# Kernel optimization log

Hardware: AMD Instinct MI355X
Metric: run time of the kernel (lower is better)

The kernel has to match this reference:

```python
import jax, jax.numpy as jnp
import numpy as np

N_NODES = 50000
N_EDGES = 800000
IN_DIM = 128
HIDDEN_DIMS = [128, 128]
OUT_DIM = 4
NUM_GRAPHS = 128


def setup_inputs() -> dict:
    key = jax.random.key(0)
    ks = jax.random.split(key, 12)
    inp = {
        "x": jax.random.normal(ks[0], (N_NODES, IN_DIM), dtype=jnp.float32),
        "edge_index": jax.random.randint(ks[1], (2, N_EDGES), 0, N_NODES, dtype=jnp.int64),
        "edge_attr": jax.random.uniform(ks[2], (N_EDGES,), dtype=jnp.float32),
        "edge_weight": jax.random.uniform(ks[3], (N_EDGES,), dtype=jnp.float32),
        "batch": jnp.sort(jax.random.randint(ks[4], (N_NODES,), 0, NUM_GRAPHS, dtype=jnp.int64)),
    }
    # GCNConv weights (Glorot-ish scale) and biases
    d_in = IN_DIM
    for i, d_out in enumerate(HIDDEN_DIMS):
        inp[f"W{i}"] = jax.random.normal(ks[5 + i], (d_in, d_out), dtype=jnp.float32) / np.sqrt(d_in)
        inp[f"b{i}"] = jnp.zeros((d_out,), dtype=jnp.float32)
        d_in = d_out
    # classifier: Linear(d,d) -> ReLU -> Linear(d,4)
    inp["Wc1"] = jax.random.normal(ks[8], (d_in, d_in), dtype=jnp.float32) / np.sqrt(d_in)
    inp["bc1"] = jnp.zeros((d_in,), dtype=jnp.float32)
    inp["Wc2"] = jax.random.normal(ks[9], (d_in, OUT_DIM), dtype=jnp.float32) / np.sqrt(d_in)
    inp["bc2"] = jnp.zeros((OUT_DIM,), dtype=jnp.float32)
    return inp


def _gcn_conv(x, src, dst, ew, W, b):
    # PyG GCNConv with add_self_loops=True, symmetric normalization.
    n = x.shape[0]
    loop = jnp.arange(n, dtype=src.dtype)
    s = jnp.concatenate([src, loop])
    d = jnp.concatenate([dst, loop])
    w = jnp.concatenate([ew, jnp.ones((n,), dtype=ew.dtype)])
    deg = jax.ops.segment_sum(w, d, num_segments=n)
    dinv = jnp.where(deg > 0, jax.lax.rsqrt(jnp.maximum(deg, 1e-12)), 0.0)
    norm = dinv[s] * w * dinv[d]  # [E+N]
    h = x @ W                     # [N, d_out] dense GEMM
    out = jax.ops.segment_sum(h[s] * norm[:, None], d, num_segments=n)
    return out + b


def reference(x, edge_index, edge_attr, edge_weight, batch,
              W0, b0, W1, b1, Wc1, bc1, Wc2, bc2):
    # NOTE: original code passes edge_attr into GCNConv's edge_weight slot;
    # edge_weight is unused. Dropout is identity (eval mode).
    src, dst = edge_index[0], edge_index[1]
    h = x
    for W, b in ((W0, b0), (W1, b1)):
        h = _gcn_conv(h, src, dst, edge_attr, W, b)
        h = jax.nn.relu(h)
    # global mean pool over graphs
    sums = jax.ops.segment_sum(h, batch, num_segments=NUM_GRAPHS)
    cnts = jax.ops.segment_sum(jnp.ones((h.shape[0],), h.dtype), batch, num_segments=NUM_GRAPHS)
    g = sums / jnp.maximum(cnts, 1.0)[:, None]  # [G, d]
    # classifier MLP
    g = jax.nn.relu(g @ Wc1 + bc1)
    return g @ Wc2 + bc2  # [G, 4]
```

## Files before the change

kernel.cpp:

```cpp
#include <hip/hip_runtime.h>
#include <hip/hip_fp16.h>

#define N_NODES 50000
#define N_EDGES 800000
#define DIM 128
#define NUM_GRAPHS 128
#define STRIDE 64

#define ATTR_SCALE 33554432.0f
#define ATTR_MASK  ((1ull << 40) - 1)

typedef _Float16 f16x8 __attribute__((ext_vector_type(8)));
typedef float f32x4 __attribute__((ext_vector_type(4)));


__global__ __launch_bounds__(256) void k_build(const int* __restrict__ src,
                                               const int* __restrict__ dst,
                                               const float* __restrict__ attr,
                                               const float* __restrict__ W0,
                                               const float* __restrict__ W1,
                                               unsigned long long* packed,
                                               unsigned int* __restrict__ epack,
                                               _Float16* __restrict__ Wt0,
                                               _Float16* __restrict__ Wt1,
                                               int E, int nbChunks) {
    int b = blockIdx.x;
    if (b >= nbChunks * 8) {
        int idx = (b - nbChunks * 8) * 256 + threadIdx.x;
        int m = idx >> 14;
        int rem = idx & 16383;
        int n = rem >> 7;
        int k = rem & 127;
        const float* W = m ? W1 : W0;
        _Float16* Wt = m ? Wt1 : Wt0;
        Wt[(size_t)n * 128 + k] = (_Float16)W[(size_t)k * 128 + n];
        return;
    }
    int slice = b & 7;
    int e = (b >> 3) * 256 + threadIdx.x;
    if (e >= E) return;
    int d = dst[e];
    if ((d & 7) != slice) return;
    float a = attr[e];
    unsigned long long add =
        (1ull << 40) | (unsigned long long)(unsigned int)(a * ATTR_SCALE + 0.5f);
    unsigned long long old = atomicAdd(&packed[d], add);
    int rank = (int)(old >> 40);
    if (rank < STRIDE) {
        __half ha = __float2half_rn(a);
        unsigned short us = *reinterpret_cast<unsigned short*>(&ha);
        epack[d * STRIDE + rank] = ((unsigned int)us << 16) | (unsigned int)src[e];
    }
}


template <typename AT>
__global__ __launch_bounds__(256) void k_gemm_mfma(const AT* __restrict__ A,
                                                   const _Float16* __restrict__ Wt,
                                                   const unsigned long long* __restrict__ packed,
                                                   __half* __restrict__ H, int n) {
    int tid = threadIdx.x;
    int w = tid >> 6, lane = tid & 63;
    int n15 = lane & 15, quad = lane >> 4;
    int node = blockIdx.x * 64 + w * 16 + n15;
    int nodec = node < n ? node : n - 1;
    const AT* Arow = A + (size_t)nodec * DIM;

    f32x4 acc[8];
#pragma unroll
    for (int t = 0; t < 8; t++) acc[t] = (f32x4){0.f, 0.f, 0.f, 0.f};

#pragma unroll
    for (int c = 0; c < 4; c++) {
        f16x8 bf;
        if constexpr (__is_same(AT, float)) {
            float4 a0 = ((const float4*)Arow)[c * 8 + quad * 2];
            float4 a1 = ((const float4*)Arow)[c * 8 + quad * 2 + 1];
            bf[0] = (_Float16)a0.x; bf[1] = (_Float16)a0.y;
            bf[2] = (_Float16)a0.z; bf[3] = (_Float16)a0.w;
            bf[4] = (_Float16)a1.x; bf[5] = (_Float16)a1.y;
            bf[6] = (_Float16)a1.z; bf[7] = (_Float16)a1.w;
        } else {
            bf = *(const f16x8*)(Arow + c * 32 + quad * 8);
        }
#pragma unroll
        for (int t = 0; t < 8; t++) {
            f16x8 af = *(const f16x8*)(Wt + (size_t)(t * 16 + n15) * 128 + c * 32 + quad * 8);
            acc[t] = __builtin_amdgcn_mfma_f32_16x16x32_f16(af, bf, acc[t], 0, 0, 0);
        }
    }

    if (node < n) {
        unsigned long long pk = packed[nodec];
        float dv = rsqrtf(1.0f + (float)(pk & ATTR_MASK) * (1.0f / ATTR_SCALE));
        __half* hp = H + (size_t)node * DIM + quad * 4;
#pragma unroll
        for (int t = 0; t < 8; t++) {
            __half2 h01 = __floats2half2_rn(acc[t][0] * dv, acc[t][1] * dv);
            __half2 h23 = __floats2half2_rn(acc[t][2] * dv, acc[t][3] * dv);
            uint2 pkd;
            pkd.x = *reinterpret_cast<unsigned int*>(&h01);
            pkd.y = *reinterpret_cast<unsigned int*>(&h23);
            *(uint2*)(hp + t * 16) = pkd;
        }
    }
}


__device__ __forceinline__ float2 unpack_h2(unsigned int u) {
    __half2 h = *reinterpret_cast<__half2*>(&u);
    return __half22float2(h);
}

template <bool POOL>
__global__ __launch_bounds__(256) void k_gather(const __half* __restrict__ H,
                                                const unsigned long long* __restrict__ packed,
                                                const unsigned int* __restrict__ epack,
                                                const float* __restrict__ bias,
                                                const int* __restrict__ batch,
                                                __half* __restrict__ OUT,
                                                float* gsum, float* cnt, int n) {
    __shared__ float lpool[8 * 128];
    __shared__ int sg[8];

    int idx = blockIdx.x * 256 + threadIdx.x;
    int i = idx >> 5;
    int lane = idx & 31;
    int w = threadIdx.x >> 5;
    const uint2* H8 = (const uint2*)H;

    unsigned long long pk = packed[i];
    int cntE = (int)(pk >> 40);
    if (cntE > STRIDE) cntE = STRIDE;
    float dv = rsqrtf(1.0f + (float)(pk & ATTR_MASK) * (1.0f / ATTR_SCALE));

    uint2 selfraw = H8[(size_t)i * 32 + lane];
    float2 s01 = unpack_h2(selfraw.x);
    float2 s23 = unpack_h2(selfraw.y);
    float4 acc = make_float4(s01.x, s01.y, s23.x, s23.y);

    int j0 = i * STRIDE;
    int end = j0 + cntE;

    for (int j = j0; j < end; j += 8) {
        int s[8];
        float wt[8];
#pragma unroll
        for (int k = 0; k < 8; k++) {
            int jj = j + k;
            bool valid = jj < end;
            int jc = valid ? jj : (end - 1);
            unsigned int pe = epack[jc];
            s[k] = (int)(pe & 0xffffu);
            __half_raw hr;
            hr.x = (unsigned short)(pe >> 16);
            float wv = __half2float(__half(hr));
            wt[k] = valid ? wv : 0.f;
        }
        uint2 v[8];
#pragma unroll
        for (int k = 0; k < 8; k++) v[k] = H8[(size_t)s[k] * 32 + lane];
#pragma unroll
        for (int k = 0; k < 8; k++) {
            float2 f01 = unpack_h2(v[k].x);
            float2 f23 = unpack_h2(v[k].y);
            acc.x += wt[k] * f01.x;
            acc.y += wt[k] * f01.y;
            acc.z += wt[k] * f23.x;
            acc.w += wt[k] * f23.y;
        }
    }

    float4 bb = ((const float4*)bias)[lane];
    acc.x = fmaxf(acc.x * dv + bb.x, 0.f);
    acc.y = fmaxf(acc.y * dv + bb.y, 0.f);
    acc.z = fmaxf(acc.z * dv + bb.z, 0.f);
    acc.w = fmaxf(acc.w * dv + bb.w, 0.f);

    if (POOL) {
        int g = batch[i];
        if (lane == 0) sg[w] = g;
        __syncthreads();
        bool uniform = true;
#pragma unroll
        for (int k = 0; k < 8; k++) uniform = uniform && (sg[k] == sg[0]);
        if (uniform) {
            ((float4*)(lpool + w * 128))[lane] = acc;
            __syncthreads();
            int t = threadIdx.x;
            if (t < 128) {
                float s = 0.f;
#pragma unroll
                for (int k = 0; k < 8; k++) s += lpool[k * 128 + t];
                atomicAdd(&gsum[sg[0] * DIM + t], s);
            }
            if (t == 0) atomicAdd(&cnt[sg[0]], 8.0f);
        } else {
            float* o = gsum + (size_t)g * DIM + lane * 4;
            atomicAdd(o + 0, acc.x);
            atomicAdd(o + 1, acc.y);
            atomicAdd(o + 2, acc.z);
            atomicAdd(o + 3, acc.w);
            if (lane == 0) atomicAdd(&cnt[g], 1.0f);
        }
    } else {
        __half2 p01 = __floats2half2_rn(acc.x, acc.y);
        __half2 p23 = __floats2half2_rn(acc.z, acc.w);
        uint2 o;
        o.x = *reinterpret_cast<unsigned int*>(&p01);
        o.y = *reinterpret_cast<unsigned int*>(&p23);
        ((uint2*)OUT)[(size_t)i * 32 + lane] = o;
    }
}


__global__ __launch_bounds__(128) void k_classifier(const float* __restrict__ gsum,
                                                    const float* __restrict__ cnt,
                                                    const float* __restrict__ Wc1,
                                                    const float* __restrict__ bc1,
                                                    const float* __restrict__ Wc2,
                                                    const float* __restrict__ bc2,
                                                    float* __restrict__ out) {
    int g = blockIdx.x;
    int t = threadIdx.x;
    __shared__ float gv[128];
    __shared__ float hid[128];
    float inv = 1.0f / fmaxf(cnt[g], 1.0f);
    gv[t] = gsum[(size_t)g * DIM + t] * inv;
    __syncthreads();
    float acc = bc1[t];
    for (int k = 0; k < 128; k++) acc += gv[k] * Wc1[k * 128 + t];
    hid[t] = fmaxf(acc, 0.f);
    __syncthreads();
    if (t < 4) {
        float o = bc2[t];
        for (int k = 0; k < 128; k++) o += hid[k] * Wc2[k * 4 + t];
        out[g * 4 + t] = o;
    }
}


extern "C" void kernel_launch(void* const* d_in, const int* in_sizes, int n_in,
                              void* d_out, int out_size, void* d_ws, size_t ws_size,
                              hipStream_t stream) {
    const float* x     = (const float*)d_in[0];
    const int*   ei    = (const int*)d_in[1];
    const float* attr  = (const float*)d_in[2];
    const int*   batch = (const int*)d_in[4];
    const float* W0  = (const float*)d_in[5];
    const float* b0  = (const float*)d_in[6];
    const float* W1  = (const float*)d_in[7];
    const float* b1  = (const float*)d_in[8];
    const float* Wc1 = (const float*)d_in[9];
    const float* bc1 = (const float*)d_in[10];
    const float* Wc2 = (const float*)d_in[11];
    const float* bc2 = (const float*)d_in[12];
    float* out = (float*)d_out;

    char* ws = (char*)d_ws;
    __half*             bufH16 = (__half*)(ws + 0);
    __half*             bufA16 = (__half*)(ws + 12800000);
    unsigned int*       epack  = (unsigned int*)(ws + 25600000);
    unsigned long long* packed = (unsigned long long*)(ws + 38400000);
    float*              gsum   = (float*)(ws + 38800000);
    float*              cnt    = (float*)(ws + 38865536);
    _Float16*           Wt0    = (_Float16*)(ws + 38866048);
    _Float16*           Wt1    = (_Float16*)(ws + 38898816);

    const int* src = ei;
    const int* dst = ei + N_EDGES;

    const int NB_C = (N_EDGES + 255) / 256;
    const int NB_G = (N_NODES * 32 + 255) / 256;
    const int NB_M = (N_NODES + 63) / 64;

    (void)hipMemsetAsync(ws + 38400000, 0, 466048, stream);

    k_build<<<NB_C * 8 + 128, 256, 0, stream>>>(src, dst, attr, W0, W1, packed,
                                                epack, Wt0, Wt1, N_EDGES, NB_C);

    k_gemm_mfma<float><<<NB_M, 256, 0, stream>>>(x, Wt0, packed, bufH16, N_NODES);
    k_gather<false><<<NB_G, 256, 0, stream>>>(bufH16, packed, epack, b0,
                                              batch, bufA16, gsum, cnt, N_NODES);

    k_gemm_mfma<_Float16><<<NB_M, 256, 0, stream>>>((const _Float16*)bufA16, Wt1,
                                                    packed, bufH16, N_NODES);
    k_gather<true><<<NB_G, 256, 0, stream>>>(bufH16, packed, epack, b1,
                                             batch, nullptr, gsum, cnt, N_NODES);

    k_classifier<<<NUM_GRAPHS, 128, 0, stream>>>(gsum, cnt, Wc1, bc1, Wc2, bc2, out);
}
```

Baseline: 273.4 us.

## Split gather columns across 4 blocks, 8 lanes per node, two-group pooling

Each block now handles 32 nodes and one quarter of the feature columns, so 8 lanes cover a node's 64-byte column slice instead of 32 lanes covering the full row. The column-group blocks for the same nodes can run on different CUs, and each warp now serves 8 nodes at once, which changes gather locality and the amount of work per thread. Pooling now handles up to two graph ids per block through shared-memory reductions, with a per-node atomic fallback for anything else. Each gather gather is now only 64 contiguous bytes per node row, and the extra syncs and block count add overhead.

```diff
diff --git a/kernel.cpp b/kernel.cpp
--- a/kernel.cpp
+++ b/kernel.cpp
@@ -120,26 +120,27 @@
                                                 const int* __restrict__ batch,
                                                 __half* __restrict__ OUT,
                                                 float* gsum, float* cnt, int n) {
-    __shared__ float lpool[8 * 128];
-    __shared__ int sg[8];
-
-    int idx = blockIdx.x * 256 + threadIdx.x;
-    int i = idx >> 5;
-    int lane = idx & 31;
-    int w = threadIdx.x >> 5;
+    int cg = blockIdx.x & 3;
+    int nb = blockIdx.x >> 2;
+    int slot = threadIdx.x >> 3;
+    int ln = threadIdx.x & 7;
+    int i = nb * 32 + slot;
+    bool valid = i < n;
+    int ic = valid ? i : n - 1;
+    int colq = cg * 8 + ln;
     const uint2* H8 = (const uint2*)H;
 
-    unsigned long long pk = packed[i];
-    int cntE = (int)(pk >> 40);
+    unsigned long long pk = packed[ic];
+    int cntE = valid ? (int)(pk >> 40) : 0;
     if (cntE > STRIDE) cntE = STRIDE;
     float dv = rsqrtf(1.0f + (float)(pk & ATTR_MASK) * (1.0f / ATTR_SCALE));
 
-    uint2 selfraw = H8[(size_t)i * 32 + lane];
+    uint2 selfraw = H8[(size_t)ic * 32 + colq];
     float2 s01 = unpack_h2(selfraw.x);
     float2 s23 = unpack_h2(selfraw.y);
     float4 acc = make_float4(s01.x, s01.y, s23.x, s23.y);
 
-    int j0 = i * STRIDE;
+    int j0 = ic * STRIDE;
     int end = j0 + cntE;
 
     for (int j = j0; j < end; j += 8) {
@@ -148,18 +149,17 @@
 #pragma unroll
         for (int k = 0; k < 8; k++) {
             int jj = j + k;
-            bool valid = jj < end;
-            int jc = valid ? jj : (end - 1);
+            bool v2 = jj < end;
+            int jc = v2 ? jj : (end - 1);
             unsigned int pe = epack[jc];
             s[k] = (int)(pe & 0xffffu);
             __half_raw hr;
             hr.x = (unsigned short)(pe >> 16);
-            float wv = __half2float(__half(hr));
-            wt[k] = valid ? wv : 0.f;
+            wt[k] = v2 ? __half2float(__half(hr)) : 0.f;
         }
         uint2 v[8];
 #pragma unroll
-        for (int k = 0; k < 8; k++) v[k] = H8[(size_t)s[k] * 32 + lane];
+        for (int k = 0; k < 8; k++) v[k] = H8[(size_t)s[k] * 32 + colq];
 #pragma unroll
         for (int k = 0; k < 8; k++) {
             float2 f01 = unpack_h2(v[k].x);
@@ -171,45 +171,77 @@
         }
     }
 
-    float4 bb = ((const float4*)bias)[lane];
+    float4 bb = ((const float4*)bias)[colq];
     acc.x = fmaxf(acc.x * dv + bb.x, 0.f);
     acc.y = fmaxf(acc.y * dv + bb.y, 0.f);
     acc.z = fmaxf(acc.z * dv + bb.z, 0.f);
     acc.w = fmaxf(acc.w * dv + bb.w, 0.f);
 
-    if (POOL) {
-        int g = batch[i];
-        if (lane == 0) sg[w] = g;
+    if constexpr (POOL) {
+        __shared__ float lpool[32 * 32];
+        __shared__ int sg[32];
+        __shared__ int meta[4];
+        if (ln == 0) sg[slot] = valid ? batch[ic] : -1;
         __syncthreads();
-        bool uniform = true;
-#pragma unroll
-        for (int k = 0; k < 8; k++) uniform = uniform && (sg[k] == sg[0]);
-        if (uniform) {
-            ((float4*)(lpool + w * 128))[lane] = acc;
+        if (threadIdx.x == 0) {
+            int nv = n - nb * 32; if (nv > 32) nv = 32;
+            int gA = sg[0];
+            int gB = sg[nv - 1];
+            int cA = 0, cB = 0;
+            for (int k2 = 0; k2 < nv; k2++) {
+                if (sg[k2] == gA) cA++;
+                else if (sg[k2] == gB) cB++;
+            }
+            meta[0] = gA; meta[1] = gB; meta[2] = cA; meta[3] = cB;
+        }
+        __syncthreads();
+        int gA = meta[0], gB = meta[1];
+        int myg = valid ? sg[slot] : -2;
+
+        bool inA = valid && (myg == gA);
+        ((float4*)(lpool + slot * 32))[ln] =
+            inA ? acc : make_float4(0.f, 0.f, 0.f, 0.f);
+        __syncthreads();
+        if (threadIdx.x < 32) {
+            float ssum = 0.f;
+#pragma unroll
+            for (int k2 = 0; k2 < 32; k2++) ssum += lpool[k2 * 32 + threadIdx.x];
+            atomicAdd(&gsum[gA * DIM + cg * 32 + threadIdx.x], ssum);
+        }
+        if (threadIdx.x == 0 && cg == 0) atomicAdd(&cnt[gA], (float)meta[2]);
+
+        if (gB != gA) {
             __syncthreads();
-            int t = threadIdx.x;
-            if (t < 128) {
-                float s = 0.f;
-#pragma unroll
-                for (int k = 0; k < 8; k++) s += lpool[k * 128 + t];
-                atomicAdd(&gsum[sg[0] * DIM + t], s);
+            bool inB = valid && (myg == gB);
+            ((float4*)(lpool + slot * 32))[ln] =
+                inB ? acc : make_float4(0.f, 0.f, 0.f, 0.f);
+            __syncthreads();
+            if (threadIdx.x < 32) {
+                float ssum = 0.f;
+#pragma unroll
+                for (int k2 = 0; k2 < 32; k2++) ssum += lpool[k2 * 32 + threadIdx.x];
+                atomicAdd(&gsum[gB * DIM + cg * 32 + threadIdx.x], ssum);
             }
-            if (t == 0) atomicAdd(&cnt[sg[0]], 8.0f);
-        } else {
-            float* o = gsum + (size_t)g * DIM + lane * 4;
+            if (threadIdx.x == 0 && cg == 0) atomicAdd(&cnt[gB], (float)meta[3]);
+        }
+
+        if (valid && myg != gA && myg != gB) {
+            float* o = gsum + (size_t)myg * DIM + cg * 32 + ln * 4;
             atomicAdd(o + 0, acc.x);
             atomicAdd(o + 1, acc.y);
             atomicAdd(o + 2, acc.z);
             atomicAdd(o + 3, acc.w);
-            if (lane == 0) atomicAdd(&cnt[g], 1.0f);
+            if (ln == 0 && cg == 0) atomicAdd(&cnt[myg], 1.0f);
         }
     } else {
-        __half2 p01 = __floats2half2_rn(acc.x, acc.y);
-        __half2 p23 = __floats2half2_rn(acc.z, acc.w);
-        uint2 o;
-        o.x = *reinterpret_cast<unsigned int*>(&p01);
-        o.y = *reinterpret_cast<unsigned int*>(&p23);
-        ((uint2*)OUT)[(size_t)i * 32 + lane] = o;
+        if (valid) {
+            __half2 p01 = __floats2half2_rn(acc.x, acc.y);
+            __half2 p23 = __floats2half2_rn(acc.z, acc.w);
+            uint2 o;
+            o.x = *reinterpret_cast<unsigned int*>(&p01);
+            o.y = *reinterpret_cast<unsigned int*>(&p23);
+            ((uint2*)OUT)[(size_t)i * 32 + colq] = o;
+        }
     }
 }
 
@@ -271,7 +303,7 @@
     const int* dst = ei + N_EDGES;
 
     const int NB_C = (N_EDGES + 255) / 256;
-    const int NB_G = (N_NODES * 32 + 255) / 256;
+    const int NB_G = ((N_NODES + 31) / 32) * 4;
     const int NB_M = (N_NODES + 63) / 64;
 
     (void)hipMemsetAsync(ws + 38400000, 0, 466048, stream);
```

New measurement: 271.0 us, median of 2. Within noise of the previous version (-0.9%).
